# Optimization experiments

Hardware: AMD Instinct MI355X
Metric: run time of the kernel (lower is better)

## Reference

```python
import jax, jax.numpy as jnp
import numpy as np

N = 100000       # num nodes
E = 1600000      # num edges
IN_DIM = 128
HID = 128
HEADS = 4
HEAD_DIM = HID // HEADS  # 32
NEG_SLOPE = 0.2
LN_EPS = 1e-5


def _glorot(key, shape):
    fan_in, fan_out = shape[-1], shape[0]
    limit = float(np.sqrt(6.0 / (fan_in + fan_out)))
    return jax.random.uniform(key, shape, jnp.float32, -limit, limit)


def setup_inputs() -> dict:
    key = jax.random.key(0)
    ks = jax.random.split(key, 16)
    return {
        "x": jax.random.normal(ks[0], (N, IN_DIM), jnp.float32),
        "edge_index": jax.random.randint(ks[1], (2, E), 0, N, jnp.int64),
        # embedding Linear(IN_DIM -> HID)
        "W_emb": _glorot(ks[2], (HID, IN_DIM)),
        "b_emb": jnp.zeros((HID,), jnp.float32),
        # E8 layer weight (F.linear, no bias)
        "W_e8": _glorot(ks[3], (HID, HID)),
        # GATConv: lin weight [HID, HEADS*HEAD_DIM], attention vectors, output bias
        "W_gat": _glorot(ks[4], (HEADS * HEAD_DIM, HID)),
        "att_src": _glorot(ks[5], (HEADS, HEAD_DIM)),
        "att_dst": _glorot(ks[6], (HEADS, HEAD_DIM)),
        "b_gat": jnp.zeros((HEADS * HEAD_DIM,), jnp.float32),
        # fusion Linear(2*HID -> HID)
        "W_fus": _glorot(ks[7], (HID, 2 * HID)),
        "b_fus": jnp.zeros((HID,), jnp.float32),
        # LayerNorm(HID)
        "gamma": jnp.ones((HID,), jnp.float32),
        "beta": jnp.zeros((HID,), jnp.float32),
        # readout MLP HID -> HID//2 -> 1
        "W_r1": _glorot(ks[8], (HID // 2, HID)),
        "b_r1": jnp.zeros((HID // 2,), jnp.float32),
        "W_r2": _glorot(ks[9], (1, HID // 2)),
        "b_r2": jnp.zeros((1,), jnp.float32),
    }


def reference(x, edge_index, W_emb, b_emb, W_e8, W_gat, att_src, att_dst,
              b_gat, W_fus, b_fus, gamma, beta, W_r1, b_r1, W_r2, b_r2):
    row = edge_index[0]  # src
    col = edge_index[1]  # dst

    # embedding
    h = x @ W_emb.T + b_emb          # [N, HID]
    res = h

    # --- E8: sparse normalized-adjacency matmul + linear ---
    deg = jax.ops.segment_sum(jnp.ones((E,), h.dtype), col, num_segments=N)
    dinv = jnp.where(deg > 0, deg ** -0.5, 0.0)
    vals = dinv[row] * dinv[col]                       # [E]
    agg = jax.ops.segment_sum(h[col] * vals[:, None], row, num_segments=N)
    x_e8 = agg @ W_e8.T                                # [N, HID]

    # --- GATConv (heads=4, concat, add_self_loops) ---
    loop = jnp.arange(N, dtype=row.dtype)
    src = jnp.concatenate([row, loop])                 # [E+N]
    dst = jnp.concatenate([col, loop])
    g = (h @ W_gat.T).reshape(N, HEADS, HEAD_DIM)      # [N, H, C]
    a_src = (g * att_src).sum(-1)                      # [N, H]
    a_dst = (g * att_dst).sum(-1)
    e = jax.nn.leaky_relu(a_src[src] + a_dst[dst], NEG_SLOPE)  # [E+N, H]
    m = jax.ops.segment_max(e, dst, num_segments=N)    # scatter-softmax max
    e = jnp.exp(e - m[dst])
    s = jax.ops.segment_sum(e, dst, num_segments=N)
    alpha = e / (s[dst] + 1e-16)                       # [E+N, H]
    msg = g[src] * alpha[..., None]                    # [E+N, H, C]
    x_gat = jax.ops.segment_sum(msg, dst, num_segments=N).reshape(N, HEADS * HEAD_DIM) + b_gat

    # --- fusion + residual + LayerNorm + ReLU ---
    f = jnp.concatenate([x_e8, x_gat], axis=-1) @ W_fus.T + b_fus
    z = f + res
    mu = z.mean(-1, keepdims=True)
    var = ((z - mu) ** 2).mean(-1, keepdims=True)
    z = (z - mu) * jax.lax.rsqrt(var + LN_EPS) * gamma + beta
    z = jax.nn.relu(z)  # dropout is identity in eval mode

    # --- readout MLP + sigmoid ---
    r = jax.nn.relu(z @ W_r1.T + b_r1)
    out = jax.nn.sigmoid(r @ W_r2.T + b_r2)            # [N, 1]
    return out
```

## Files before the change

### kernel.cpp

```cpp
#include <hip/hip_runtime.h>
#include <hip/hip_bf16.h>
#include <math.h>

#define NWIN 8
#define NCHUNK 256
#define CAP 64

typedef __attribute__((ext_vector_type(8))) short bf16x8;
typedef __attribute__((ext_vector_type(4))) float f32x4;

__device__ __forceinline__ float us2f(unsigned short u) {
    return __uint_as_float(((unsigned)u) << 16);
}
__device__ __forceinline__ unsigned short f2bf(float f) {
    unsigned u = __float_as_uint(f);
    u += 0x7FFF + ((u >> 16) & 1);
    return (unsigned short)(u >> 16);
}

__global__ void setup_kernel(const float* __restrict__ b_gat, const float* __restrict__ W_fus,
                             const float* __restrict__ b_fus, float* __restrict__ bfus2,
                             const float* __restrict__ We, const float* __restrict__ W8,
                             const float* __restrict__ Wg, unsigned short* __restrict__ W16,
                             int* __restrict__ cnt, int total) {
    int b = blockIdx.x;
    if (b == 0) {
        int t = threadIdx.x;
        if (t < 128) {
            float acc = b_fus[t];
            for (int k = 0; k < 128; k++)
                acc += b_gat[k] * W_fus[t * 256 + 128 + k];
            bfus2[t] = acc;
        }
        return;
    }
    if (b <= 320) {
        int i = (b - 1) * 256 + threadIdx.x;
        if (i < 81920) {
            float v;
            if (i < 16384) v = We[i];
            else if (i < 32768) v = W8[i - 16384];
            else if (i < 49152) v = Wg[i - 32768];
            else v = W_fus[i - 49152];
            W16[i] = f2bf(v);
        }
        return;
    }
    int i = (b - 321) * 256 + threadIdx.x;
    if (i < total) cnt[i] = 0;
}

__device__ __forceinline__ void fill_body(
    int bid, const int* __restrict__ row, const int* __restrict__ col,
    int* __restrict__ cnt, int* __restrict__ adjF, int E, int N, int win) {
    int w = bid & (NWIN - 1);
    int chunk = bid >> 3;
    int lo = w * win, hi = lo + win;
    int per = (E + NCHUNK - 1) / NCHUNK;
    per = (per + 1) & ~1;
    int s = chunk * per;
    int e_end = s + per; if (e_end > E) e_end = E;

    for (int i = s + (int)threadIdx.x * 2; i < e_end; i += 512) {
        int2 rv, cv;
        if (i + 1 < e_end) {
            rv = *(const int2*)(row + i);
            cv = *(const int2*)(col + i);
        } else {
            rv.x = row[i]; rv.y = -1;
            cv.x = col[i]; cv.y = 0;
        }
        if (cv.x >= lo && cv.x < hi) {
            int p = atomicAdd(&cnt[cv.x], 1);
            if (p < CAP) adjF[(size_t)cv.x * CAP + p] = rv.x;
        }
        int k2 = N + rv.x;
        if (k2 >= lo && k2 < hi) {
            int p = atomicAdd(&cnt[k2], 1);
            if (p < CAP) adjF[(size_t)k2 * CAP + p] = cv.x;
        }
        if (rv.y >= 0) {
            if (cv.y >= lo && cv.y < hi) {
                int p = atomicAdd(&cnt[cv.y], 1);
                if (p < CAP) adjF[(size_t)cv.y * CAP + p] = rv.y;
            }
            int k3 = N + rv.y;
            if (k3 >= lo && k3 < hi) {
                int p = atomicAdd(&cnt[k3], 1);
                if (p < CAP) adjF[(size_t)k3 * CAP + p] = cv.y;
            }
        }
    }
}

template <bool A_FP32, bool HAS_BIAS, bool OUT_F32, bool OUT_BF16, bool OUT_ATT>
__device__ __forceinline__ void gemm_body(
    int bid, const void* __restrict__ A_, const unsigned short* __restrict__ W16,
    const float* __restrict__ bias, float* __restrict__ Cf,
    unsigned short* __restrict__ C16,
    const float* __restrict__ attS, const float* __restrict__ attD,
    float* __restrict__ aS, float* __restrict__ aD, int n) {
    const int t = threadIdx.x;
    const int wave = t >> 6, lane = t & 63;
    const int quad = lane >> 4, ln = lane & 15;
    const int row0 = bid * 128 + wave * 32;
    const int kq = quad * 8;

    f32x4 zero = {0.f, 0.f, 0.f, 0.f};
    f32x4 acc[2][8];
#pragma unroll
    for (int i = 0; i < 2; i++)
#pragma unroll
        for (int j = 0; j < 8; j++) acc[i][j] = zero;

#pragma unroll
    for (int ks = 0; ks < 4; ks++) {
        bf16x8 a[2];
#pragma unroll
        for (int mt = 0; mt < 2; mt++) {
            int row = row0 + mt * 16 + ln;
            if (row >= n) row = n - 1;
            if (A_FP32) {
                const float* ap = (const float*)A_ + (size_t)row * 128 + ks * 32 + kq;
                float4 f0 = *(const float4*)ap;
                float4 f1 = *(const float4*)(ap + 4);
                bf16x8 v;
                v[0] = (short)f2bf(f0.x); v[1] = (short)f2bf(f0.y);
                v[2] = (short)f2bf(f0.z); v[3] = (short)f2bf(f0.w);
                v[4] = (short)f2bf(f1.x); v[5] = (short)f2bf(f1.y);
                v[6] = (short)f2bf(f1.z); v[7] = (short)f2bf(f1.w);
                a[mt] = v;
            } else {
                a[mt] = *(const bf16x8*)((const unsigned short*)A_ +
                                         (size_t)row * 128 + ks * 32 + kq);
            }
        }
#pragma unroll
        for (int nt = 0; nt < 8; nt++) {
            bf16x8 b = *(const bf16x8*)(W16 + (size_t)(nt * 16 + ln) * 128 + ks * 32 + kq);
            acc[0][nt] = __builtin_amdgcn_mfma_f32_16x16x32_bf16(a[0], b, acc[0][nt], 0, 0, 0);
            acc[1][nt] = __builtin_amdgcn_mfma_f32_16x16x32_bf16(a[1], b, acc[1][nt], 0, 0, 0);
        }
    }

    float bv[8];
    if (HAS_BIAS) {
#pragma unroll
        for (int nt = 0; nt < 8; nt++) bv[nt] = bias[nt * 16 + ln];
    }
    float asv[8], adv[8];
    if (OUT_ATT) {
#pragma unroll
        for (int nt = 0; nt < 8; nt++) {
            int idx = (nt >> 1) * 32 + (nt & 1) * 16 + ln;
            asv[nt] = attS[idx];
            adv[nt] = attD[idx];
        }
    }
#pragma unroll
    for (int mt = 0; mt < 2; mt++) {
        int rbase = row0 + mt * 16 + quad * 4;
#pragma unroll
        for (int reg = 0; reg < 4; reg++) {
            int row = rbase + reg;
            if (row >= n) continue;
            if (OUT_ATT) {
                float ps[4] = {0.f, 0.f, 0.f, 0.f};
                float pd[4] = {0.f, 0.f, 0.f, 0.f};
#pragma unroll
                for (int nt = 0; nt < 8; nt++) {
                    float v = acc[mt][nt][reg];
                    ps[nt >> 1] += v * asv[nt];
                    pd[nt >> 1] += v * adv[nt];
                }
#pragma unroll
                for (int m = 1; m < 16; m <<= 1) {
#pragma unroll
                    for (int hh = 0; hh < 4; hh++) {
                        ps[hh] += __shfl_xor(ps[hh], m);
                        pd[hh] += __shfl_xor(pd[hh], m);
                    }
                }
                if (ln == 0) {
                    *(float4*)&aS[(size_t)row * 4] = make_float4(ps[0], ps[1], ps[2], ps[3]);
                    *(float4*)&aD[(size_t)row * 4] = make_float4(pd[0], pd[1], pd[2], pd[3]);
                }
            }
#pragma unroll
            for (int nt = 0; nt < 8; nt++) {
                float v = acc[mt][nt][reg];
                if (HAS_BIAS) v += bv[nt];
                int col = nt * 16 + ln;
                if (OUT_F32) Cf[(size_t)row * 128 + col] = v;
                if (OUT_BF16) C16[(size_t)row * 128 + col] = f2bf(v);
            }
        }
    }
}

__global__ __launch_bounds__(256) void fill_emb_kernel(
    const float* __restrict__ x, const unsigned short* __restrict__ We16,
    const float* __restrict__ b_emb, float* __restrict__ hf,
    const int* __restrict__ row, const int* __restrict__ col,
    int* __restrict__ cnt, int* __restrict__ adjF, int E, int N, int win, int GB) {
    int b = blockIdx.x;
    if (b < GB)
        gemm_body<true, true, true, false, false>(b, x, We16, b_emb, hf, nullptr,
                                                  nullptr, nullptr, nullptr, nullptr, N);
    else
        fill_body(b - GB, row, col, cnt, adjF, E, N, win);
}

template <bool A_FP32, bool HAS_BIAS, bool OUT_F32, bool OUT_BF16, bool OUT_ATT>
__global__ __launch_bounds__(256) void gemm_kernel(
    const void* __restrict__ A_, const unsigned short* __restrict__ W16,
    const float* __restrict__ bias, float* __restrict__ Cf,
    unsigned short* __restrict__ C16,
    const float* __restrict__ attS, const float* __restrict__ attD,
    float* __restrict__ aS, float* __restrict__ aD, int n) {
    gemm_body<A_FP32, HAS_BIAS, OUT_F32, OUT_BF16, OUT_ATT>(
        blockIdx.x, A_, W16, bias, Cf, C16, attS, attD, aS, aD, n);
}

__device__ __forceinline__ void e8_body(
    int bid, const int* __restrict__ cnt, const int* __restrict__ adjF,
    const float* __restrict__ hf, unsigned short* __restrict__ agg16, int N) {
    int r = bid * 4 + ((int)threadIdx.x >> 6);
    int lane = threadIdx.x & 63;
    if (r >= N) return;
    int key = N + r;
    int m = min(cnt[key], CAP);
    int av = (lane < m) ? adjF[(size_t)key * CAP + lane] : 0;
    float ax = 0.f, ay = 0.f;
    int j = 0;
    for (; j + 8 <= m; j += 8) {
        int c[8]; int dc[8]; float2 hv[8];
#pragma unroll
        for (int q = 0; q < 8; q++) c[q] = __shfl(av, j + q);
#pragma unroll
        for (int q = 0; q < 8; q++) dc[q] = cnt[c[q]];
#pragma unroll
        for (int q = 0; q < 8; q++)
            hv[q] = *(const float2*)&hf[(size_t)c[q] * 128 + lane * 2];
#pragma unroll
        for (int q = 0; q < 8; q++) {
            float dv = rsqrtf((float)dc[q]);
            ax += hv[q].x * dv;
            ay += hv[q].y * dv;
        }
    }
    for (; j < m; j++) {
        int c = __shfl(av, j);
        float dv = rsqrtf((float)cnt[c]);
        float2 hv = *(const float2*)&hf[(size_t)c * 128 + lane * 2];
        ax += hv.x * dv;
        ay += hv.y * dv;
    }
    int dcr = cnt[r];
    float dr = dcr > 0 ? rsqrtf((float)dcr) : 0.f;
    ushort2 o; o.x = f2bf(ax * dr); o.y = f2bf(ay * dr);
    *(ushort2*)&agg16[(size_t)r * 128 + lane * 2] = o;
}

__device__ __forceinline__ void gat_body(
    int bid, const int* __restrict__ cnt, const int* __restrict__ adjF,
    const float* __restrict__ a_src, const float* __restrict__ a_dst,
    const unsigned short* __restrict__ g16, unsigned short* __restrict__ xg16,
    int N, float* __restrict__ wlds) {
    int d = bid * 4 + ((int)threadIdx.x >> 6);
    int lane = threadIdx.x & 63;
    int wave = threadIdx.x >> 6;
    if (d >= N) return;
    float* wl = wlds + wave * 272;

    float4 ad4 = *(const float4*)&a_dst[(size_t)d * 4];
    float4 asd = *(const float4*)&a_src[(size_t)d * 4];
    float adh[4] = {ad4.x, ad4.y, ad4.z, ad4.w};
    float tS[4] = {asd.x + ad4.x, asd.y + ad4.y, asd.z + ad4.z, asd.w + ad4.w};
#pragma unroll
    for (int h = 0; h < 4; h++) tS[h] = tS[h] > 0.f ? tS[h] : 0.2f * tS[h];

    int mm = min(cnt[d], CAP);
    int av = (lane < mm) ? adjF[(size_t)d * CAP + lane] : 0;

    float t[4];
    if (lane < mm) {
        float4 a4 = *(const float4*)&a_src[(size_t)av * 4];
        float ta[4] = {a4.x, a4.y, a4.z, a4.w};
#pragma unroll
        for (int h = 0; h < 4; h++) {
            float e = ta[h] + adh[h];
            t[h] = e > 0.f ? e : 0.2f * e;
        }
    } else {
#pragma unroll
        for (int h = 0; h < 4; h++) t[h] = -3e38f;
    }
    float m[4];
#pragma unroll
    for (int h = 0; h < 4; h++) m[h] = t[h];
#pragma unroll
    for (int off = 1; off < 64; off <<= 1) {
#pragma unroll
        for (int h = 0; h < 4; h++) m[h] = fmaxf(m[h], __shfl_xor(m[h], off));
    }
#pragma unroll
    for (int h = 0; h < 4; h++) m[h] = fmaxf(m[h], tS[h]);

    float w_[4], l[4];
#pragma unroll
    for (int h = 0; h < 4; h++) {
        w_[h] = (lane < mm) ? __expf(t[h] - m[h]) : 0.f;
        l[h] = w_[h];
    }
#pragma unroll
    for (int off = 1; off < 64; off <<= 1) {
#pragma unroll
        for (int h = 0; h < 4; h++) l[h] += __shfl_xor(l[h], off);
    }
    float wS[4];
#pragma unroll
    for (int h = 0; h < 4; h++) {
        wS[h] = __expf(tS[h] - m[h]);
        l[h] += wS[h];
        wl[h * 68 + lane] = w_[h];
    }

    int hd = lane >> 4;
    ushort2 g0 = *(const ushort2*)&g16[(size_t)d * 128 + lane * 2];
    float accx = wS[hd] * us2f(g0.x), accy = wS[hd] * us2f(g0.y);
    const float* wh = wl + hd * 68;
    int j = 0;
    for (; j + 8 <= mm; j += 8) {
        int s[8]; float wv[8]; ushort2 gu[8];
#pragma unroll
        for (int q = 0; q < 8; q++) s[q] = __shfl(av, j + q);
#pragma unroll
        for (int q = 0; q < 8; q++) wv[q] = wh[j + q];
#pragma unroll
        for (int q = 0; q < 8; q++)
            gu[q] = *(const ushort2*)&g16[(size_t)s[q] * 128 + lane * 2];
#pragma unroll
        for (int q = 0; q < 8; q++) {
            accx += wv[q] * us2f(gu[q].x);
            accy += wv[q] * us2f(gu[q].y);
        }
    }
    for (; j < mm; j++) {
        int s = __shfl(av, j);
        float wv = wh[j];
        ushort2 gu = *(const ushort2*)&g16[(size_t)s * 128 + lane * 2];
        accx += wv * us2f(gu.x);
        accy += wv * us2f(gu.y);
    }
    float inv = 1.f / l[hd];
    ushort2 o; o.x = f2bf(accx * inv); o.y = f2bf(accy * inv);
    *(ushort2*)&xg16[(size_t)d * 128 + lane * 2] = o;
}

__global__ __launch_bounds__(256) void e8gat_kernel(
    const int* __restrict__ cnt, const int* __restrict__ adjF,
    const float* __restrict__ hf, unsigned short* __restrict__ agg16,
    const float* __restrict__ a_src, const float* __restrict__ a_dst,
    const unsigned short* __restrict__ g16, unsigned short* __restrict__ xg16, int N) {
    __shared__ float wlds[4 * 272];
    int b = blockIdx.x;
    if (b & 1) gat_body(b >> 1, cnt, adjF, a_src, a_dst, g16, xg16, N, wlds);
    else       e8_body(b >> 1, cnt, adjF, hf, agg16, N);
}

__global__ __launch_bounds__(256) void fusion_ln_mfma(
    const unsigned short* __restrict__ xe816, const unsigned short* __restrict__ xg16,
    const unsigned short* __restrict__ Wf16,
    const float* __restrict__ bfus2, const float* __restrict__ hf,
    const float* __restrict__ gamma, const float* __restrict__ beta,
    float* __restrict__ zf, int n) {
    const int t = threadIdx.x;
    const int wave = t >> 6, lane = t & 63;
    const int quad = lane >> 4, ln = lane & 15;
    const int row0 = blockIdx.x * 128 + wave * 32;
    const int kq = quad * 8;

    f32x4 zero = {0.f, 0.f, 0.f, 0.f};
    f32x4 acc[2][8];
#pragma unroll
    for (int i = 0; i < 2; i++)
#pragma unroll
        for (int j = 0; j < 8; j++) acc[i][j] = zero;

    for (int half = 0; half < 2; half++) {
        const unsigned short* A = half ? xg16 : xe816;
#pragma unroll
        for (int ks = 0; ks < 4; ks++) {
            bf16x8 a[2];
#pragma unroll
            for (int mt = 0; mt < 2; mt++) {
                int row = row0 + mt * 16 + ln;
                if (row >= n) row = n - 1;
                a[mt] = *(const bf16x8*)(A + (size_t)row * 128 + ks * 32 + kq);
            }
#pragma unroll
            for (int nt = 0; nt < 8; nt++) {
                bf16x8 b = *(const bf16x8*)(Wf16 + (size_t)(nt * 16 + ln) * 256 +
                                            half * 128 + ks * 32 + kq);
                acc[0][nt] = __builtin_amdgcn_mfma_f32_16x16x32_bf16(a[0], b, acc[0][nt], 0, 0, 0);
                acc[1][nt] = __builtin_amdgcn_mfma_f32_16x16x32_bf16(a[1], b, acc[1][nt], 0, 0, 0);
            }
        }
    }

    float bv[8], gm[8], bt[8];
#pragma unroll
    for (int nt = 0; nt < 8; nt++) {
        int c = nt * 16 + ln;
        bv[nt] = bfus2[c]; gm[nt] = gamma[c]; bt[nt] = beta[c];
    }
#pragma unroll
    for (int mt = 0; mt < 2; mt++) {
#pragma unroll
        for (int reg = 0; reg < 4; reg++) {
            int row = row0 + mt * 16 + quad * 4 + reg;
            if (row >= n) continue;
            float v[8];
            float s1 = 0.f, s2 = 0.f;
#pragma unroll
            for (int nt = 0; nt < 8; nt++) {
                float x = acc[mt][nt][reg] + bv[nt] + hf[(size_t)row * 128 + nt * 16 + ln];
                v[nt] = x; s1 += x; s2 += x * x;
            }
#pragma unroll
            for (int m = 1; m < 16; m <<= 1) {
                s1 += __shfl_xor(s1, m);
                s2 += __shfl_xor(s2, m);
            }
            float mu = s1 * (1.f / 128.f);
            float var = s2 * (1.f / 128.f) - mu * mu;
            float inv = rsqrtf(var + 1e-5f);
#pragma unroll
            for (int nt = 0; nt < 8; nt++) {
                float o = (v[nt] - mu) * inv * gm[nt] + bt[nt];
                o = o > 0.f ? o : 0.f;
                zf[(size_t)row * 128 + nt * 16 + ln] = o;
            }
        }
    }
}

__global__ __launch_bounds__(256) void readout_kernel(
    const float* __restrict__ z, const float* __restrict__ W1,
    const float* __restrict__ b1, const float* __restrict__ W2,
    const float* __restrict__ b2, float* __restrict__ out, int N) {
    __shared__ float zs[32 * 132];
    __shared__ float wlds[64 * 132];
    __shared__ float w2s[64];
    __shared__ float b1s[64];
    const int t = threadIdx.x;
    const int row0 = blockIdx.x * 32;

    for (int i = 0; i < 4; i++) {
        int idx = i * 256 + t;
        int r = idx >> 5, c4 = idx & 31;
        float4 v = make_float4(0.f, 0.f, 0.f, 0.f);
        if (row0 + r < N) v = *(const float4*)&z[(size_t)(row0 + r) * 128 + c4 * 4];
        *(float4*)&zs[r * 132 + c4 * 4] = v;
    }
    for (int i = 0; i < 8; i++) {
        int idx = i * 256 + t;
        int o = idx >> 5, c4 = idx & 31;
        *(float4*)&wlds[o * 132 + c4 * 4] = *(const float4*)&W1[o * 128 + c4 * 4];
    }
    if (t < 64) { w2s[t] = W2[t]; b1s[t] = b1[t]; }
    __syncthreads();

    const int rg = t >> 4;
    const int cg = t & 15;
    float acc[2][4] = {};
    const float* z0 = &zs[(rg * 2) * 132];
    const float* z1 = z0 + 132;
    for (int k4 = 0; k4 < 32; k4++) {
        float4 a0 = *(const float4*)&z0[k4 * 4];
        float4 a1 = *(const float4*)&z1[k4 * 4];
#pragma unroll
        for (int j = 0; j < 4; j++) {
            float4 wv = *(const float4*)&wlds[(cg * 4 + j) * 132 + k4 * 4];
            acc[0][j] += a0.x * wv.x + a0.y * wv.y + a0.z * wv.z + a0.w * wv.w;
            acc[1][j] += a1.x * wv.x + a1.y * wv.y + a1.z * wv.z + a1.w * wv.w;
        }
    }
    float p0 = 0.f, p1 = 0.f;
#pragma unroll
    for (int j = 0; j < 4; j++) {
        int o = cg * 4 + j;
        float r0 = acc[0][j] + b1s[o]; r0 = r0 > 0.f ? r0 : 0.f;
        float r1 = acc[1][j] + b1s[o]; r1 = r1 > 0.f ? r1 : 0.f;
        p0 += r0 * w2s[o]; p1 += r1 * w2s[o];
    }
    for (int off = 8; off > 0; off >>= 1) {
        p0 += __shfl_down(p0, off, 16);
        p1 += __shfl_down(p1, off, 16);
    }
    if (cg == 0) {
        float bb = b2[0];
        int r0i = row0 + rg * 2, r1i = r0i + 1;
        if (r0i < N) out[r0i] = 1.f / (1.f + __expf(-(p0 + bb)));
        if (r1i < N) out[r1i] = 1.f / (1.f + __expf(-(p1 + bb)));
    }
}

extern "C" void kernel_launch(void* const* d_in, const int* in_sizes, int n_in,
                              void* d_out, int out_size, void* d_ws, size_t ws_size,
                              hipStream_t stream) {
    const float* x     = (const float*)d_in[0];
    const int*   ei    = (const int*)d_in[1];
    const float* W_emb = (const float*)d_in[2];
    const float* b_emb = (const float*)d_in[3];
    const float* W_e8  = (const float*)d_in[4];
    const float* W_gat = (const float*)d_in[5];
    const float* att_s = (const float*)d_in[6];
    const float* att_d = (const float*)d_in[7];
    const float* b_gat = (const float*)d_in[8];
    const float* W_fus = (const float*)d_in[9];
    const float* b_fus = (const float*)d_in[10];
    const float* gamma = (const float*)d_in[11];
    const float* beta  = (const float*)d_in[12];
    const float* W_r1  = (const float*)d_in[13];
    const float* b_r1  = (const float*)d_in[14];
    const float* W_r2  = (const float*)d_in[15];
    const float* b_r2  = (const float*)d_in[16];

    const int N = in_sizes[0] / 128;
    const int E = in_sizes[1] / 2;
    const int* rowp = ei;
    const int* colp = ei + E;
    const int total = 2 * N;
    const int win = (total + NWIN - 1) / NWIN;
    const int GB = (N + 127) / 128;
    const int GATB = (N + 3) / 4;

    const size_t NF = (size_t)N * 128;
    char* base = (char*)d_ws;
    float*          hf    = (float*)base;
    unsigned short* bufA  = (unsigned short*)(hf + NF);
    unsigned short* xe816 = bufA + NF;
    unsigned short* g16   = xe816 + NF;
    unsigned short* xg16  = g16 + NF;
    int*            adjF  = (int*)(xg16 + NF);
    float*          zf    = (float*)adjF;
    float* a_src = (float*)(adjF + NF);
    float* a_dst = a_src + (size_t)4 * N;
    float* bfus2 = a_dst + (size_t)4 * N;
    unsigned short* W16a = (unsigned short*)(bfus2 + 128);
    unsigned short* We16 = W16a;
    unsigned short* W816 = W16a + 16384;
    unsigned short* Wg16 = W16a + 32768;
    unsigned short* Wf16 = W16a + 49152;
    int* cnt = (int*)(W16a + 81920);

    int setup_grid = 321 + (total + 255) / 256;
    setup_kernel<<<setup_grid, 256, 0, stream>>>(b_gat, W_fus, b_fus, bfus2,
                                                 W_emb, W_e8, W_gat, W16a, cnt, total);

    fill_emb_kernel<<<GB + NWIN * NCHUNK, 256, 0, stream>>>(
        x, We16, b_emb, hf, rowp, colp, cnt, adjF, E, N, win, GB);

    gemm_kernel<true, false, false, true, true><<<GB, 256, 0, stream>>>(
        hf, Wg16, nullptr, nullptr, g16, att_s, att_d, a_src, a_dst, N);

    e8gat_kernel<<<2 * GATB, 256, 0, stream>>>(
        cnt, adjF, hf, bufA, a_src, a_dst, g16, xg16, N);

    gemm_kernel<false, false, false, true, false><<<GB, 256, 0, stream>>>(
        bufA, W816, nullptr, nullptr, xe816, nullptr, nullptr, nullptr, nullptr, N);

    fusion_ln_mfma<<<GB, 256, 0, stream>>>(xe816, xg16, Wf16, bfus2, hf,
                                           gamma, beta, zf, N);

    readout_kernel<<<(N + 31) / 32, 256, 0, stream>>>(zf, W_r1, b_r1, W_r2, b_r2,
                                                      (float*)d_out, N);
}
```

Baseline: 645.6 us.

## Fold W_gat into W_emb to compute GAT projection directly from x

Precomputes the composed weight W_gat·W_emb and bias W_gat·b_emb in the setup kernel. The GAT projection and attention scores are then computed from x in the same fused block as the embedding GEMM, so the separate GEMM launch over hf is gone. This trades a second read of hf for a second read of x within the same block, and adds a small weight-product computation at setup. Rounding changes slightly because the composed weight is stored in bf16.

```diff
diff --git a/kernel.cpp b/kernel.cpp
--- a/kernel.cpp
+++ b/kernel.cpp
@@ -21,29 +21,38 @@
 __global__ void setup_kernel(const float* __restrict__ b_gat, const float* __restrict__ W_fus,
                              const float* __restrict__ b_fus, float* __restrict__ bfus2,
                              const float* __restrict__ We, const float* __restrict__ W8,
-                             const float* __restrict__ Wg, unsigned short* __restrict__ W16,
+                             const float* __restrict__ Wg, const float* __restrict__ b_emb,
+                             float* __restrict__ bg, unsigned short* __restrict__ W16,
                              int* __restrict__ cnt, int total) {
     int b = blockIdx.x;
     if (b == 0) {
         int t = threadIdx.x;
         if (t < 128) {
             float acc = b_fus[t];
-            for (int k = 0; k < 128; k++)
+            float accg = 0.f;
+            for (int k = 0; k < 128; k++) {
                 acc += b_gat[k] * W_fus[t * 256 + 128 + k];
+                accg += Wg[t * 128 + k] * b_emb[k];
+            }
             bfus2[t] = acc;
+            bg[t] = accg;
         }
         return;
     }
+    if (b <= 256) {
+        int i = (b - 1) * 256 + threadIdx.x;
+        if (i < 16384) W16[i] = f2bf(We[i]);
+        else if (i < 32768) W16[i] = f2bf(W8[i - 16384]);
+        else W16[49152 + (i - 32768)] = f2bf(W_fus[i - 32768]);
+        return;
+    }
     if (b <= 320) {
-        int i = (b - 1) * 256 + threadIdx.x;
-        if (i < 81920) {
-            float v;
-            if (i < 16384) v = We[i];
-            else if (i < 32768) v = W8[i - 16384];
-            else if (i < 49152) v = Wg[i - 32768];
-            else v = W_fus[i - 49152];
-            W16[i] = f2bf(v);
-        }
+        int idx = (b - 257) * 256 + threadIdx.x;
+        int o = idx >> 7, k = idx & 127;
+        float acc = 0.f;
+        for (int j = 0; j < 128; j++)
+            acc += Wg[o * 128 + j] * We[j * 128 + k];
+        W16[32768 + idx] = f2bf(acc);
         return;
     }
     int i = (b - 321) * 256 + threadIdx.x;
@@ -164,14 +173,20 @@
         for (int reg = 0; reg < 4; reg++) {
             int row = rbase + reg;
             if (row >= n) continue;
+            float vv[8];
+#pragma unroll
+            for (int nt = 0; nt < 8; nt++) {
+                float v = acc[mt][nt][reg];
+                if (HAS_BIAS) v += bv[nt];
+                vv[nt] = v;
+            }
             if (OUT_ATT) {
                 float ps[4] = {0.f, 0.f, 0.f, 0.f};
                 float pd[4] = {0.f, 0.f, 0.f, 0.f};
 #pragma unroll
                 for (int nt = 0; nt < 8; nt++) {
-                    float v = acc[mt][nt][reg];
-                    ps[nt >> 1] += v * asv[nt];
-                    pd[nt >> 1] += v * adv[nt];
+                    ps[nt >> 1] += vv[nt] * asv[nt];
+                    pd[nt >> 1] += vv[nt] * adv[nt];
                 }
 #pragma unroll
                 for (int m = 1; m < 16; m <<= 1) {
@@ -188,27 +203,32 @@
             }
 #pragma unroll
             for (int nt = 0; nt < 8; nt++) {
-                float v = acc[mt][nt][reg];
-                if (HAS_BIAS) v += bv[nt];
                 int col = nt * 16 + ln;
-                if (OUT_F32) Cf[(size_t)row * 128 + col] = v;
-                if (OUT_BF16) C16[(size_t)row * 128 + col] = f2bf(v);
-            }
-        }
-    }
-}
-
-__global__ __launch_bounds__(256) void fill_emb_kernel(
+                if (OUT_F32) Cf[(size_t)row * 128 + col] = vv[nt];
+                if (OUT_BF16) C16[(size_t)row * 128 + col] = f2bf(vv[nt]);
+            }
+        }
+    }
+}
+
+__global__ __launch_bounds__(256) void fill_embg_kernel(
     const float* __restrict__ x, const unsigned short* __restrict__ We16,
     const float* __restrict__ b_emb, float* __restrict__ hf,
+    const unsigned short* __restrict__ Wge16, const float* __restrict__ bg,
+    unsigned short* __restrict__ g16,
+    const float* __restrict__ attS, const float* __restrict__ attD,
+    float* __restrict__ aS, float* __restrict__ aD,
     const int* __restrict__ row, const int* __restrict__ col,
     int* __restrict__ cnt, int* __restrict__ adjF, int E, int N, int win, int GB) {
     int b = blockIdx.x;
-    if (b < GB)
-        gemm_body<true, true, true, false, false>(b, x, We16, b_emb, hf, nullptr,
-                                                  nullptr, nullptr, nullptr, nullptr, N);
-    else
+    if (b < GB) {
+        gemm_body<true, true, true, false, false>(
+            b, x, We16, b_emb, hf, nullptr, nullptr, nullptr, nullptr, nullptr, N);
+        gemm_body<true, true, false, true, true>(
+            b, x, Wge16, bg, nullptr, g16, attS, attD, aS, aD, N);
+    } else {
         fill_body(b - GB, row, col, cnt, adjF, E, N, win);
+    }
 }
 
 template <bool A_FP32, bool HAS_BIAS, bool OUT_F32, bool OUT_BF16, bool OUT_ATT>
@@ -549,22 +569,22 @@
     float* a_src = (float*)(adjF + NF);
     float* a_dst = a_src + (size_t)4 * N;
     float* bfus2 = a_dst + (size_t)4 * N;
-    unsigned short* W16a = (unsigned short*)(bfus2 + 128);
-    unsigned short* We16 = W16a;
-    unsigned short* W816 = W16a + 16384;
-    unsigned short* Wg16 = W16a + 32768;
-    unsigned short* Wf16 = W16a + 49152;
+    float* bg    = bfus2 + 128;
+    unsigned short* W16a  = (unsigned short*)(bg + 128);
+    unsigned short* We16  = W16a;
+    unsigned short* W816  = W16a + 16384;
+    unsigned short* Wge16 = W16a + 32768;
+    unsigned short* Wf16  = W16a + 49152;
     int* cnt = (int*)(W16a + 81920);
 
     int setup_grid = 321 + (total + 255) / 256;
     setup_kernel<<<setup_grid, 256, 0, stream>>>(b_gat, W_fus, b_fus, bfus2,
-                                                 W_emb, W_e8, W_gat, W16a, cnt, total);
-
-    fill_emb_kernel<<<GB + NWIN * NCHUNK, 256, 0, stream>>>(
-        x, We16, b_emb, hf, rowp, colp, cnt, adjF, E, N, win, GB);
-
-    gemm_kernel<true, false, false, true, true><<<GB, 256, 0, stream>>>(
-        hf, Wg16, nullptr, nullptr, g16, att_s, att_d, a_src, a_dst, N);
+                                                 W_emb, W_e8, W_gat, b_emb, bg,
+                                                 W16a, cnt, total);
+
+    fill_embg_kernel<<<GB + NWIN * NCHUNK, 256, 0, stream>>>(
+        x, We16, b_emb, hf, Wge16, bg, g16, att_s, att_d, a_src, a_dst,
+        rowp, colp, cnt, adjF, E, N, win, GB);
 
     e8gat_kernel<<<2 * GATB, 256, 0, stream>>>(
         cnt, adjF, hf, bufA, a_src, a_dst, g16, xg16, N);
```

After: 650.9 us. No clear change (+0.8%).
